# Kernel optimization log

Measured on AMD Instinct MI355X. Metric: run time of the kernel, lower is better.

The kernel has to match this reference:

```python
import jax, jax.numpy as jnp
import numpy as np

B, C, H, W = 32, 1, 720, 1280


def setup_inputs() -> dict:
    key = jax.random.key(0)
    k1, k2 = jax.random.split(key)
    right_img = jax.random.normal(k1, (B, C, H, W), dtype=jnp.float32)
    # disparity in [0, 64): realistic stereo disparities, some pixels sample out of bounds
    disp = jax.random.uniform(k2, (B, C, H, W), dtype=jnp.float32) * 64.0
    return {"right_img": right_img, "disp": disp}


def _warp(right_img, disp):
    b, c, h, w = right_img.shape
    dt = disp.dtype
    # grid construction (align_corners=True style normalization, as in the module)
    xs = jnp.arange(w, dtype=dt)  # [W]
    ys = jnp.arange(h, dtype=dt)  # [H]
    gx = xs[None, None, :] - disp[:, 0]                      # [B,H,W]
    gx = (gx - (w - 1) / 2) / (w - 1) * 2
    gy = (ys[None, :, None] - (h - 1) / 2) / (h - 1) * 2     # [1,H,1]
    gy = jnp.broadcast_to(gy, gx.shape)                      # [B,H,W]
    # F.grid_sample default: bilinear, align_corners=False, padding_mode='zeros'
    ix = ((gx + 1) * w - 1) / 2
    iy = ((gy + 1) * h - 1) / 2
    x0 = jnp.floor(ix)
    y0 = jnp.floor(iy)
    wx1 = ix - x0
    wy1 = iy - y0
    wx0 = 1.0 - wx1
    wy0 = 1.0 - wy1
    x0i = x0.astype(jnp.int32)
    y0i = y0.astype(jnp.int32)
    x1i = x0i + 1
    y1i = y0i + 1

    def gather(img, yy, xx):  # img [C,H,W]; yy,xx [H,W] -> [C,H,W]
        valid = (xx >= 0) & (xx < w) & (yy >= 0) & (yy < h)
        xc = jnp.clip(xx, 0, w - 1)
        yc = jnp.clip(yy, 0, h - 1)
        return img[:, yc, xc] * valid[None].astype(img.dtype)

    g = jax.vmap(gather)
    v00 = g(right_img, y0i, x0i)
    v01 = g(right_img, y0i, x1i)
    v10 = g(right_img, y1i, x0i)
    v11 = g(right_img, y1i, x1i)
    out = (v00 * (wy0 * wx0)[:, None] + v01 * (wy0 * wx1)[:, None]
           + v10 * (wy1 * wx0)[:, None] + v11 * (wy1 * wx1)[:, None])
    return out  # [B,C,H,W]


def reference(right_img, disp):
    return _warp(right_img, disp)
```

## Files before the change

kernel.cpp:

```cpp
#include <hip/hip_runtime.h>

constexpr int Bn = 32;
constexpr int Hn = 720;
constexpr int Wn = 1280;

__global__ __launch_bounds__(256) void warp_kernel(
    const float* __restrict__ img,
    const float* __restrict__ disp,
    float* __restrict__ out)
{
    const int hw = Hn * Wn;
    const long long total4 = (long long)Bn * hw / 4;
    long long t = (long long)blockIdx.x * blockDim.x + threadIdx.x;
    if (t >= total4) return;
    long long base = t * 4;

    int b   = (int)(base / hw);
    int rem = (int)(base % hw);
    int y   = rem / Wn;
    int x   = rem - y * Wn;

    float gy  = (((float)y - (float)(Hn - 1) * 0.5f) / (float)(Hn - 1)) * 2.0f;
    float iy  = ((gy + 1.0f) * (float)Hn - 1.0f) * 0.5f;
    float fy0 = floorf(iy);
    float wy1 = iy - fy0;
    float wy0 = 1.0f - wy1;
    int   y0  = (int)fy0;
    int   y1  = y0 + 1;
    bool  vy0 = (y0 >= 0) && (y0 < Hn);
    bool  vy1 = (y1 >= 0) && (y1 < Hn);
    int   y0c = min(max(y0, 0), Hn - 1);
    int   y1c = min(max(y1, 0), Hn - 1);

    const float* __restrict__ imb  = img + (long long)b * hw;
    const float* __restrict__ row0 = imb + (long long)y0c * Wn;
    const float* __restrict__ row1 = imb + (long long)y1c * Wn;

    const float4 d4 = *reinterpret_cast<const float4*>(disp + base);
    float dv[4] = {d4.x, d4.y, d4.z, d4.w};
    float res[4];

#pragma unroll
    for (int i = 0; i < 4; ++i) {
        float xf  = (float)(x + i);
        float gx  = ((xf - dv[i] - (float)(Wn - 1) * 0.5f) / (float)(Wn - 1)) * 2.0f;
        float ix  = ((gx + 1.0f) * (float)Wn - 1.0f) * 0.5f;
        float fx0 = floorf(ix);
        float wx1 = ix - fx0;
        float wx0 = 1.0f - wx1;
        int   x0  = (int)fx0;
        int   x1  = x0 + 1;
        bool  vx0 = (x0 >= 0) && (x0 < Wn);
        bool  vx1 = (x1 >= 0) && (x1 < Wn);
        int   x0c = min(max(x0, 0), Wn - 1);
        int   x1c = min(max(x1, 0), Wn - 1);

        float m00 = (vy0 && vx0) ? 1.0f : 0.0f;
        float m01 = (vy0 && vx1) ? 1.0f : 0.0f;
        float m10 = (vy1 && vx0) ? 1.0f : 0.0f;
        float m11 = (vy1 && vx1) ? 1.0f : 0.0f;

        float v00 = row0[x0c] * m00;
        float v01 = row0[x1c] * m01;
        float v10 = row1[x0c] * m10;
        float v11 = row1[x1c] * m11;

        res[i] = v00 * (wy0 * wx0) + v01 * (wy0 * wx1)
               + v10 * (wy1 * wx0) + v11 * (wy1 * wx1);
    }

    float4 o4 = make_float4(res[0], res[1], res[2], res[3]);
    *reinterpret_cast<float4*>(out + base) = o4;
}

extern "C" void kernel_launch(void* const* d_in, const int* in_sizes, int n_in,
                              void* d_out, int out_size, void* d_ws, size_t ws_size,
                              hipStream_t stream) {
    const float* img  = (const float*)d_in[0];
    const float* disp = (const float*)d_in[1];
    float* out = (float*)d_out;

    const long long total4 = (long long)Bn * Hn * Wn / 4;
    const int block = 256;
    const int grid  = (int)((total4 + block - 1) / block);

    warp_kernel<<<grid, block, 0, stream>>>(img, disp, out);
}
```

Baseline: 299.6 us.

## Stage the two source rows in shared memory, one block per output row

Each block now handles one output row (320 threads × 4 pixels) and first cooperatively loads the two needed source image rows into LDS with float4 loads, then performs the gathers from shared memory instead of global memory. This removes scattered global gathers in exchange for a block-wide barrier and an extra row load per block. The rows are largely reused across neighbouring output rows, so global traffic may rise slightly, but the gathers become LDS reads.

```diff
diff --git a/kernel.cpp b/kernel.cpp
--- a/kernel.cpp
+++ b/kernel.cpp
@@ -4,21 +4,18 @@
 constexpr int Hn = 720;
 constexpr int Wn = 1280;
 
-__global__ __launch_bounds__(256) void warp_kernel(
+__global__ __launch_bounds__(320) void warp_kernel(
     const float* __restrict__ img,
     const float* __restrict__ disp,
     float* __restrict__ out)
 {
-    const int hw = Hn * Wn;
-    const long long total4 = (long long)Bn * hw / 4;
-    long long t = (long long)blockIdx.x * blockDim.x + threadIdx.x;
-    if (t >= total4) return;
-    long long base = t * 4;
+    __shared__ float srow[2 * Wn];
 
-    int b   = (int)(base / hw);
-    int rem = (int)(base % hw);
-    int y   = rem / Wn;
-    int x   = rem - y * Wn;
+    const int hw  = Hn * Wn;
+    const int blk = blockIdx.x;
+    const int b   = blk / Hn;
+    const int y   = blk - b * Hn;
+    const int tid = threadIdx.x;
 
     float gy  = (((float)y - (float)(Hn - 1) * 0.5f) / (float)(Hn - 1)) * 2.0f;
     float iy  = ((gy + 1.0f) * (float)Hn - 1.0f) * 0.5f;
@@ -32,17 +29,31 @@
     int   y0c = min(max(y0, 0), Hn - 1);
     int   y1c = min(max(y1, 0), Hn - 1);
 
-    const float* __restrict__ imb  = img + (long long)b * hw;
-    const float* __restrict__ row0 = imb + (long long)y0c * Wn;
-    const float* __restrict__ row1 = imb + (long long)y1c * Wn;
+    const float* __restrict__ imb = img + (long long)b * hw;
 
+    {
+        const float4* __restrict__ src0 = reinterpret_cast<const float4*>(imb + (long long)y0c * Wn);
+        const float4* __restrict__ src1 = reinterpret_cast<const float4*>(imb + (long long)y1c * Wn);
+        float4* dst = reinterpret_cast<float4*>(srow);
+        dst[tid]       = src0[tid];
+        dst[320 + tid] = src1[tid];
+    }
+    __syncthreads();
+
+    const float* __restrict__ r0 = srow;
+    const float* __restrict__ r1 = srow + Wn;
+
+    const long long base = (long long)blk * Wn + 4 * tid;
     const float4 d4 = *reinterpret_cast<const float4*>(disp + base);
     float dv[4] = {d4.x, d4.y, d4.z, d4.w};
     float res[4];
 
+    const float my0 = vy0 ? 1.0f : 0.0f;
+    const float my1 = vy1 ? 1.0f : 0.0f;
+
 #pragma unroll
     for (int i = 0; i < 4; ++i) {
-        float xf  = (float)(x + i);
+        float xf  = (float)(4 * tid + i);
         float gx  = ((xf - dv[i] - (float)(Wn - 1) * 0.5f) / (float)(Wn - 1)) * 2.0f;
         float ix  = ((gx + 1.0f) * (float)Wn - 1.0f) * 0.5f;
         float fx0 = floorf(ix);
@@ -50,20 +61,15 @@
         float wx0 = 1.0f - wx1;
         int   x0  = (int)fx0;
         int   x1  = x0 + 1;
-        bool  vx0 = (x0 >= 0) && (x0 < Wn);
-        bool  vx1 = (x1 >= 0) && (x1 < Wn);
+        float mx0 = ((x0 >= 0) && (x0 < Wn)) ? 1.0f : 0.0f;
+        float mx1 = ((x1 >= 0) && (x1 < Wn)) ? 1.0f : 0.0f;
         int   x0c = min(max(x0, 0), Wn - 1);
         int   x1c = min(max(x1, 0), Wn - 1);
 
-        float m00 = (vy0 && vx0) ? 1.0f : 0.0f;
-        float m01 = (vy0 && vx1) ? 1.0f : 0.0f;
-        float m10 = (vy1 && vx0) ? 1.0f : 0.0f;
-        float m11 = (vy1 && vx1) ? 1.0f : 0.0f;
-
-        float v00 = row0[x0c] * m00;
-        float v01 = row0[x1c] * m01;
-        float v10 = row1[x0c] * m10;
-        float v11 = row1[x1c] * m11;
+        float v00 = r0[x0c] * (my0 * mx0);
+        float v01 = r0[x1c] * (my0 * mx1);
+        float v10 = r1[x0c] * (my1 * mx0);
+        float v11 = r1[x1c] * (my1 * mx1);
 
         res[i] = v00 * (wy0 * wx0) + v01 * (wy0 * wx1)
                + v10 * (wy1 * wx0) + v11 * (wy1 * wx1);
@@ -80,9 +86,8 @@
     const float* disp = (const float*)d_in[1];
     float* out = (float*)d_out;
 
-    const long long total4 = (long long)Bn * Hn * Wn / 4;
-    const int block = 256;
-    const int grid  = (int)((total4 + block - 1) / block);
+    const int grid  = Bn * Hn;
+    const int block = 320;
 
     warp_kernel<<<grid, block, 0, stream>>>(img, disp, out);
 }
```

New measurement: 271.5 us. 9.4% less time.
